# Kernel optimization log

Hardware: AMD Instinct MI355X
Metric: run time of the kernel (lower is better)

The kernel has to match this reference:

```python
import jax, jax.numpy as jnp
import numpy as np

NG, NF, NW = 5, 10, 8
STEP = NG + NF + 1          # 16 signatures per writer
MARGIN = 1.0
MODEL_LAMBDA = 0.01
GAMMA = 5.0                 # SoftDTW gamma from the module
BIG = 1e9                   # finite 'inf' so vjp stays NaN-free


def _pairwise_sq(x):
    # x: [B, N, F] -> squared-euclidean self-distance matrices [B, N, N]
    sq = jnp.sum(x * x, axis=-1)
    return sq[:, :, None] + sq[:, None, :] - 2.0 * jnp.einsum('bnf,bmf->bnm', x, x)


def _softdtw_diag_table(D):
    # Anti-diagonal Soft-DTW DP over all B matrices at once.
    # Returns all DP diagonals Rall[k, b, i] = R[i, k-i] so we can read
    # R[L-1, L-1] for each per-signature length L.
    B, N, _ = D.shape
    ii = jnp.arange(N)
    ks = jnp.arange(2 * N - 1)
    jidx = ks[:, None] - ii[None, :]                 # [2N-1, N] column index per diag
    valid = (jidx >= 0) & (jidx < N)
    jcl = jnp.clip(jidx, 0, N - 1)
    Ddiag = D[:, ii[None, :], jcl]                   # [B, 2N-1, N]
    Ddiag = jnp.transpose(Ddiag, (1, 0, 2))          # [2N-1, B, N]
    Ddiag = jnp.where(valid[:, None, :], Ddiag, 0.0)

    def shift(v):  # shift along i (last axis), pad with BIG
        return jnp.concatenate([jnp.full_like(v[:, :1], BIG), v[:, :-1]], axis=1)

    def softmin(a, b, c):
        return -GAMMA * jax.nn.logsumexp(jnp.stack([a, b, c]) * (-1.0 / GAMMA), axis=0)

    # k = 0: only cell (0,0): R = D[0,0] (softmin(0, inf, inf) = 0)
    R0 = jnp.where(ii[None, :] == 0, Ddiag[0], BIG)  # [B, N]
    Rm2_init = jnp.full_like(R0, BIG)

    def step(carry, inp):
        Rm2, Rm1 = carry
        Dk, vk = inp
        # cell (i, k-i): deps (i-1,j-1)=Rm2[i-1], (i-1,j)=Rm1[i-1], (i,j-1)=Rm1[i]
        Rk = Dk + softmin(shift(Rm2), shift(Rm1), Rm1)
        Rk = jnp.where(vk[None, :], Rk, BIG)
        return (Rm1, Rk), Rk

    _, Rs = jax.lax.scan(step, (Rm2_init, R0), (Ddiag[1:], valid[1:]))
    return jnp.concatenate([R0[None], Rs], axis=0)   # [2N-1, B, N]


def _forward(data, lens):
    B, N, _ = data.shape
    L = jnp.clip(lens.astype(jnp.int32), 1, N)       # valid prefix length per signature
    D = _pairwise_sq(data)                           # [B, N, N]
    Rall = _softdtw_diag_table(D)                    # [2N-1, B, N]
    # sdtw(x[:L], x[:L]) == R[L-1, L-1], found on diagonal k=2L-2 at position L-1
    sdtw_self = Rall[2 * L - 2, jnp.arange(B), L - 1]
    dists = sdtw_self / (2.0 * L.astype(data.dtype))  # /(len+len)

    d = dists.reshape(NW, STEP)
    dm = (d[:, :, None] + d[:, None, :]) * 0.5       # [NW, STEP, STEP]
    g = NG + 1
    dmg = dm[:, :g, :g]
    # scores[w,j,a,b] = relu(dm[w,j,a] + margin - dm[w,j,g+b]); lks[j] = max scalar
    scores = jax.nn.relu(dmg[:, :, :, None] + MARGIN - dm[:, :g, g:][:, :, None, :])
    maxj = jnp.max(scores, axis=(2, 3))              # [NW, g]
    sum_lks = jnp.sum(maxj, axis=1) * (g * NF)       # lks[j] broadcast over (g, nf)
    nnz = jnp.sum((maxj != 0).astype(data.dtype), axis=1) * (g * NF)
    lv = sum_lks / (nnz + 1.0)
    tril = jnp.tril(jnp.ones((g, g), dtype=bool), k=-1)
    only_pos = jnp.sum(jnp.where(tril[None], dmg, 0.0), axis=(1, 2)) * (MODEL_LAMBDA / NG)
    return jnp.sum(lv + only_pos) / NW


def setup_inputs() -> dict:
    key = jax.random.key(0)
    k1, k2 = jax.random.split(key)
    B = NW * STEP                                    # 128
    data = jax.random.normal(k1, (B, 512, 32), dtype=jnp.float32)
    lens = jax.random.randint(k2, (B,), 64, 513, dtype=jnp.int32)
    return {"data": data, "lens": lens}


def reference(data, lens):
    return _forward(data, lens)
```

## Files before the change

### kernel.cpp

```cpp
#include <hip/hip_runtime.h>
#include <stdint.h>

#define NGK   5
#define NFK   10
#define NWK   8
#define STEPW 16
#define NSEQ  512
#define FDIM  32
#define NBAT  128
#define SROWS 576
#define DEPTH 12
#define NR2   319
#define BIGV  1000000000.0f

#define INVGL 0.28853900817779268f
#define GLN2  3.4657359027997265f

#define EXP2F(x) __builtin_amdgcn_exp2f(x)
#define LOG2F(x) __builtin_amdgcn_logf(x)

typedef short bf16x8 __attribute__((ext_vector_type(8)));
typedef float f32x4  __attribute__((ext_vector_type(4)));
union U32F { uint32_t u; float f; };

__device__ __forceinline__ uint32_t f2bf(float f) {
    U32F c; c.f = f;
    return (c.u + 0x7FFFu + ((c.u >> 16) & 1u)) >> 16;
}
__device__ __forceinline__ float bflo(uint32_t u) { U32F c; c.u = u << 16; return c.f; }
__device__ __forceinline__ float bfhi(uint32_t u) { U32F c; c.u = u & 0xFFFF0000u; return c.f; }

__device__ __forceinline__ float dpp_shr1_f(float v) {
    U32F c; c.f = v;
    c.u = (uint32_t)__builtin_amdgcn_update_dpp(0, (int)c.u, 0x138, 0xF, 0xF, true);
    return c.f;
}

__global__ __launch_bounds__(256, 1) void prep_kernel(
    const float* __restrict__ data, uint16_t* __restrict__ xbf,
    float* __restrict__ sq)
{
    __shared__ uint32_t LB[NSEQ * 16];
    const int b = blockIdx.x;
    const int t = threadIdx.x;
    const float4* xb4 = (const float4*)(data + (size_t)b * (NSEQ * FDIM));
    uint2* xg = (uint2*)(xbf + (size_t)b * (NSEQ * FDIM));

    #pragma unroll
    for (int it = 0; it < 16; ++it) {
        int q = it * 256 + t;
        float4 v = xb4[q];
        uint32_t u0 = f2bf(v.x) | (f2bf(v.y) << 16);
        uint32_t u1 = f2bf(v.z) | (f2bf(v.w) << 16);
        LB[q * 2] = u0; LB[q * 2 + 1] = u1;
        uint2 st; st.x = u0; st.y = u1;
        xg[q] = st;
    }
    __syncthreads();
    #pragma unroll
    for (int rr = 0; rr < 2; ++rr) {
        int r = t + rr * 256;
        float acc = 0.f;
        #pragma unroll
        for (int c = 0; c < 16; ++c) {
            uint32_t u = LB[r * 16 + c];
            float lo = bflo(u), hi = bfhi(u);
            acc = fmaf(lo, lo, acc);
            acc = fmaf(hi, hi, acc);
        }
        sq[(size_t)b * NSEQ + r] = acc;
    }
}

__global__ __launch_bounds__(256, 1) void dgen2_kernel(
    const uint16_t* __restrict__ xbf, const float* __restrict__ sq,
    const int* __restrict__ lens, uint16_t* __restrict__ wsk)
{
    const int tj = blockIdx.x, b = blockIdx.y;
    int L = lens[b]; L = L < 1 ? 1 : (L > NSEQ ? NSEQ : L);
    const int lout = (L - 1) >> 3;
    const int maxS = ((L - 1) + 2 * lout) >> 1;
    if (tj * 16 > 2 * maxS + 1) return;

    const int t = threadIdx.x;
    const int w = t >> 6, lane = t & 63, rl = lane & 15, kq = lane >> 4, rr0 = kq * 4;
    const int j = tj * 16 + rl;

    const short* xb  = (const short*)(xbf + (size_t)b * (NSEQ * FDIM));
    const float* sqb = sq + (size_t)b * NSEQ;
    uint16_t* wb = wsk + (size_t)b * (NR2 * 1024);

    bf16x8 bfrag = *(const bf16x8*)(xb + j * FDIM + kq * 8);
    float sqJ = sqb[j];
    const bool jok = j < L;
    const int q0 = rr0 & 7;
    const int ladd = rr0 >> 3;

    for (int it = 0; it < 8; ++it) {
        int ti = w * 8 + it;
        if (tj * 16 + 4 * ti > 2 * maxS + 1) break;
        bf16x8 afrag = *(const bf16x8*)(xb + (ti * 16 + rl) * FDIM + kq * 8);
        f32x4 c = {0.f, 0.f, 0.f, 0.f};
        c = __builtin_amdgcn_mfma_f32_16x16x32_bf16(afrag, bfrag, c, 0, 0, 0);
        f32x4 s4 = *(const f32x4*)(sqb + ti * 16 + rr0);
        float wv[4];
        #pragma unroll
        for (int q2 = 0; q2 < 4; ++q2) {
            int i = ti * 16 + rr0 + q2;
            float dv = s4[q2] + sqJ - 2.f * c[q2];
            float e = EXP2F(-INVGL * dv);
            wv[q2] = (jok && (i < L)) ? e : 0.f;
        }
        int l  = ti * 2 + ladd;
        int cc = j + 2 * l;
        int S  = cc >> 1, sub = cc & 1;
        if (S <= maxS) {
            uint2 st;
            st.x = f2bf(wv[0]) | (f2bf(wv[1]) << 16);
            st.y = f2bf(wv[2]) | (f2bf(wv[3]) << 16);
            *(uint2*)(wb + (size_t)S * 1024 + l * 16 + sub * 8 + q0) = st;
        }
    }
}

__global__ __launch_bounds__(64, 1) void dp2_kernel(
    const uint16_t* __restrict__ wsk, const int* __restrict__ lens,
    float* __restrict__ dists, uint32_t* __restrict__ ctr,
    float* __restrict__ out)
{
    const int b = blockIdx.x, wl = threadIdx.x;
    const uint16_t* wb = wsk + (size_t)b * (NR2 * 1024) + wl * 16;
    int L = lens[b]; L = L < 1 ? 1 : (L > NSEQ ? NSEQ : L);
    const int lout = (L - 1) >> 3, qout = (L - 1) & 7;
    const int cout = (L - 1) + 2 * lout;
    const int S_out = cout >> 1;

#define ISSUE2(QA, QB, row) {                                                 \
    int gl_ = (row); if (gl_ > NR2 - 1) gl_ = NR2 - 1;                        \
    const uint16_t* pg_ = wb + (size_t)gl_ * 1024;                            \
    asm volatile("global_load_dwordx4 %0, %2, off\n\t"                        \
                 "global_load_dwordx4 %1, %2, off offset:16"                  \
                 : "=&v"(QA), "=&v"(QB) : "v"(pg_));                          \
}

    uint4 A0r, B0r, A1r, B1r, A2r, B2r, A3r, B3r,
          A4r, B4r, A5r, B5r, A6r, B6r, A7r, B7r;
    ISSUE2(A0r, B0r, 0) ISSUE2(A1r, B1r, 1) ISSUE2(A2r, B2r, 2) ISSUE2(A3r, B3r, 3)
    ISSUE2(A4r, B4r, 4) ISSUE2(A5r, B5r, 5) ISSUE2(A6r, B6r, 6) ISSUE2(A7r, B7r, 7)

    float E0 = 0.f, E1 = 0.f, E2 = 0.f, E3 = 0.f,
          E4 = 0.f, E5 = 0.f, E6 = 0.f, E7 = 0.f;
    float f0 = 0.f, f1 = 0.f, f2 = 0.f, f3 = 0.f,
          f4 = 0.f, f5 = 0.f, f6 = 0.f, f7 = 0.f;
    float ap  = (wl == 0) ? 1.0f : 0.f;
    float f7p = 0.f;

    int s = 0;

#define DSTEP(QA, QB) {                                                       \
    asm volatile("s_waitcnt vmcnt(14)" ::: "memory");                         \
    __builtin_amdgcn_sched_barrier(0);                                        \
    float wa0 = bflo(QA.x), wa1 = bfhi(QA.x), wa2 = bflo(QA.y), wa3 = bfhi(QA.y); \
    float wa4 = bflo(QA.z), wa5 = bfhi(QA.z), wa6 = bflo(QA.w), wa7 = bfhi(QA.w); \
    float wb0 = bflo(QB.x), wb1 = bfhi(QB.x), wb2 = bflo(QB.y), wb3 = bfhi(QB.y); \
    float wb4 = bflo(QB.z), wb5 = bfhi(QB.z), wb6 = bflo(QB.w), wb7 = bfhi(QB.w); \
    ISSUE2(QA, QB, s + 8);                                                    \
    float buA = dpp_shr1_f(f7p);                                              \
    float buB = dpp_shr1_f(E7);                                               \
    float a0 = (ap + E0) * wa0, a1 = (E0 + E1) * wa1;                         \
    float a2 = (E1 + E2) * wa2, a3 = (E2 + E3) * wa3;                         \
    float a4 = (E3 + E4) * wa4, a5 = (E4 + E5) * wa5;                         \
    float a6 = (E5 + E6) * wa6, a7 = (E6 + E7) * wa7;                         \
    f0 = fmaf(buA, wa0, a0);                                                  \
    f1 = fmaf(f0, wa1, a1);                                                   \
    f2 = fmaf(f1, wa2, a2);                                                   \
    f3 = fmaf(f2, wa3, a3);                                                   \
    f4 = fmaf(f3, wa4, a4);                                                   \
    f5 = fmaf(f4, wa5, a5);                                                   \
    f6 = fmaf(f5, wa6, a6);                                                   \
    f7 = fmaf(f6, wa7, a7);                                                   \
    float b0 = (buA + f0) * wb0, b1 = (f0 + f1) * wb1;                        \
    float b2 = (f1 + f2) * wb2, b3 = (f2 + f3) * wb3;                         \
    float b4 = (f3 + f4) * wb4, b5 = (f4 + f5) * wb5;                         \
    float b6 = (f5 + f6) * wb6, b7 = (f6 + f7) * wb7;                         \
    E0 = fmaf(buB, wb0, b0);                                                  \
    E1 = fmaf(E0, wb1, b1);                                                   \
    E2 = fmaf(E1, wb2, b2);                                                   \
    E3 = fmaf(E2, wb3, b3);                                                   \
    E4 = fmaf(E3, wb4, b4);                                                   \
    E5 = fmaf(E4, wb5, b5);                                                   \
    E6 = fmaf(E5, wb6, b6);                                                   \
    E7 = fmaf(E6, wb7, b7);                                                   \
    ap = buB; f7p = f7; ++s;                                                  \
}

    for (;;) {
        DSTEP(A0r, B0r); if (s > S_out) break;
        DSTEP(A1r, B1r); if (s > S_out) break;
        DSTEP(A2r, B2r); if (s > S_out) break;
        DSTEP(A3r, B3r); if (s > S_out) break;
        DSTEP(A4r, B4r); if (s > S_out) break;
        DSTEP(A5r, B5r); if (s > S_out) break;
        DSTEP(A6r, B6r); if (s > S_out) break;
        DSTEP(A7r, B7r); if (s > S_out) break;
    }
#undef DSTEP
#undef ISSUE2
    asm volatile("s_waitcnt vmcnt(0)" ::: "memory");

    if (wl == lout) {
        float eo;
        if ((cout & 1) == 0) {
            eo = f0;
            if (qout == 1) eo = f1; if (qout == 2) eo = f2; if (qout == 3) eo = f3;
            if (qout == 4) eo = f4; if (qout == 5) eo = f5; if (qout == 6) eo = f6;
            if (qout == 7) eo = f7;
        } else {
            eo = E0;
            if (qout == 1) eo = E1; if (qout == 2) eo = E2; if (qout == 3) eo = E3;
            if (qout == 4) eo = E4; if (qout == 5) eo = E5; if (qout == 6) eo = E6;
            if (qout == 7) eo = E7;
        }
        float dv = -GLN2 * LOG2F(eo) * (0.5f / (float)L);
        __hip_atomic_store(&dists[b], dv, __ATOMIC_RELEASE, __HIP_MEMORY_SCOPE_AGENT);
    }

    int old = 0;
    if (wl == 0) {
        old = (int)__hip_atomic_fetch_add(ctr, 1u, __ATOMIC_ACQ_REL,
                                          __HIP_MEMORY_SCOPE_AGENT);
    }
    old = __shfl(old, 0);
    if (old == NBAT - 1) {
        const int g = NGK + 1;
        float part = 0.f;
        if (wl < NWK) {
            float dd[STEPW];
            #pragma unroll
            for (int s2 = 0; s2 < STEPW; ++s2)
                dd[s2] = __hip_atomic_load(&dists[wl * STEPW + s2],
                                           __ATOMIC_RELAXED, __HIP_MEMORY_SCOPE_AGENT);
            float sum_lks = 0.f, nnz = 0.f;
            for (int ii = 0; ii < g; ++ii) {
                float mx = 0.f;
                for (int jj = 0; jj < g; ++jj) {
                    float dmg_ij = 0.5f * (dd[ii] + dd[jj]);
                    for (int f = 0; f < NFK; ++f) {
                        float sc = dmg_ij + 1.0f - 0.5f * (dd[ii] + dd[g + f]);
                        sc = fmaxf(sc, 0.f);
                        mx = fmaxf(mx, sc);
                    }
                }
                sum_lks += mx;
                nnz += (mx != 0.f) ? 1.f : 0.f;
            }
            sum_lks *= (float)(g * NFK);
            nnz     *= (float)(g * NFK);
            float lv = sum_lks / (nnz + 1.f);
            float only_pos = 0.f;
            for (int ii = 1; ii < g; ++ii)
                for (int jj = 0; jj < ii; ++jj)
                    only_pos += 0.5f * (dd[ii] + dd[jj]);
            only_pos *= (0.01f / (float)NGK);
            part = lv + only_pos;
        }
        float tot = 0.f;
        #pragma unroll
        for (int w2 = 0; w2 < NWK; ++w2) tot += __shfl(part, w2);
        if (wl == 0) out[0] = tot * (1.0f / (float)NWK);
    }
}

__global__ __launch_bounds__(256, 1) void dgen_kernel(
    const uint16_t* __restrict__ xbf, const float* __restrict__ sq,
    const int* __restrict__ lens, uint16_t* __restrict__ wsk)
{
    const int tj = blockIdx.x, b = blockIdx.y;
    int L = lens[b]; L = L < 1 ? 1 : (L > NSEQ ? NSEQ : L);
    const int smax = (L - 1) + ((L - 1) >> 3);
    int maxrow = smax + 8; if (maxrow > SROWS - 1) maxrow = SROWS - 1;
    if (tj * 16 > maxrow) return;

    const int t = threadIdx.x;
    const int w = t >> 6, lane = t & 63, rl = lane & 15, kq = lane >> 4, rr0 = kq * 4;
    const int j = tj * 16 + rl;

    const short* xb  = (const short*)(xbf + (size_t)b * (NSEQ * FDIM));
    const float* sqb = sq + (size_t)b * NSEQ;
    uint16_t* wb = wsk + (size_t)b * (SROWS * NSEQ);

    bf16x8 bfrag = *(const bf16x8*)(xb + j * FDIM + kq * 8);
    float sqJ = sqb[j];
    const bool jok = j < L;

    for (int it = 0; it < 8; ++it) {
        int ti = w * 8 + it;
        if (tj * 16 + ti * 2 > maxrow) break;
        bf16x8 afrag = *(const bf16x8*)(xb + (ti * 16 + rl) * FDIM + kq * 8);
        f32x4 c = {0.f, 0.f, 0.f, 0.f};
        c = __builtin_amdgcn_mfma_f32_16x16x32_bf16(afrag, bfrag, c, 0, 0, 0);
        f32x4 s4 = *(const f32x4*)(sqb + ti * 16 + rr0);
        float wv[4];
        #pragma unroll
        for (int q2 = 0; q2 < 4; ++q2) {
            int i = ti * 16 + rr0 + q2;
            float dv = s4[q2] + sqJ - 2.f * c[q2];
            float e = EXP2F(-INVGL * dv);
            wv[q2] = (jok && (i < L)) ? e : 0.f;
        }
        int sr = j + ti * 2 + (rr0 >> 3);
        uint2 st;
        st.x = f2bf(wv[0]) | (f2bf(wv[1]) << 16);
        st.y = f2bf(wv[2]) | (f2bf(wv[3]) << 16);
        *(uint2*)(wb + (size_t)sr * NSEQ + ti * 16 + rr0) = st;
    }
}

__global__ __launch_bounds__(64, 1) void dp_kernel(
    const uint16_t* __restrict__ wsk, const int* __restrict__ lens,
    float* __restrict__ dists, uint32_t* __restrict__ ctr,
    float* __restrict__ out)
{
    const int b = blockIdx.x, wl = threadIdx.x;
    const uint16_t* wb = wsk + (size_t)b * (SROWS * NSEQ) + wl * 8;
    int L = lens[b]; L = L < 1 ? 1 : (L > NSEQ ? NSEQ : L);
    const int lout = (L - 1) >> 3, qout = (L - 1) & 7, smax = (L - 1) + lout;

#define ISSUE(Q, row) {                                                       \
    int gl_ = (row); if (gl_ > SROWS - 1) gl_ = SROWS - 1;                    \
    const uint16_t* pg_ = wb + (size_t)gl_ * NSEQ;                            \
    asm volatile("global_load_dwordx4 %0, %1, off" : "=&v"(Q) : "v"(pg_));    \
}

    uint4 Q0, Q1, Q2, Q3, Q4, Q5, Q6, Q7, Q8, Q9, Qa, Qb;
    ISSUE(Q0, 0)  ISSUE(Q1, 1)  ISSUE(Q2, 2)  ISSUE(Q3, 3)
    ISSUE(Q4, 4)  ISSUE(Q5, 5)  ISSUE(Q6, 6)  ISSUE(Q7, 7)
    ISSUE(Q8, 8)  ISSUE(Q9, 9)  ISSUE(Qa, 10) ISSUE(Qb, 11)

    float E0 = 0.f, E1 = 0.f, E2 = 0.f, E3 = 0.f,
          E4 = 0.f, E5 = 0.f, E6 = 0.f, E7 = 0.f;
    float ap = (wl == 0) ? 1.0f : 0.f;

    int s = 0;

#define PHASE(Q) {                                                            \
    asm volatile("s_waitcnt vmcnt(11)" ::: "memory");                         \
    __builtin_amdgcn_sched_barrier(0);                                        \
    float w0 = bflo(Q.x), w1 = bfhi(Q.x), w2 = bflo(Q.y), w3 = bfhi(Q.y);     \
    float w4 = bflo(Q.z), w5 = bfhi(Q.z), w6 = bflo(Q.w), w7 = bfhi(Q.w);     \
    ISSUE(Q, s + DEPTH);                                                      \
    float bu = dpp_shr1_f(E7);                                                \
    float A0 = (ap + E0) * w0, A1 = (E0 + E1) * w1;                           \
    float A2 = (E1 + E2) * w2, A3 = (E2 + E3) * w3;                           \
    float A4 = (E3 + E4) * w4, A5 = (E4 + E5) * w5;                           \
    float A6 = (E5 + E6) * w6, A7 = (E6 + E7) * w7;                           \
    E0 = fmaf(bu, w0, A0);                                                    \
    E1 = fmaf(E0, w1, A1);                                                    \
    E2 = fmaf(E1, w2, A2);                                                    \
    E3 = fmaf(E2, w3, A3);                                                    \
    E4 = fmaf(E3, w4, A4);                                                    \
    E5 = fmaf(E4, w5, A5);                                                    \
    E6 = fmaf(E5, w6, A6);                                                    \
    E7 = fmaf(E6, w7, A7);                                                    \
    ap = bu; ++s;                                                             \
}

    for (;;) {
        PHASE(Q0); if (s > smax) break;
        PHASE(Q1); if (s > smax) break;
        PHASE(Q2); if (s > smax) break;
        PHASE(Q3); if (s > smax) break;
        PHASE(Q4); if (s > smax) break;
        PHASE(Q5); if (s > smax) break;
        PHASE(Q6); if (s > smax) break;
        PHASE(Q7); if (s > smax) break;
        PHASE(Q8); if (s > smax) break;
        PHASE(Q9); if (s > smax) break;
        PHASE(Qa); if (s > smax) break;
        PHASE(Qb); if (s > smax) break;
    }
#undef PHASE
#undef ISSUE
    asm volatile("s_waitcnt vmcnt(0)" ::: "memory");

    if (wl == lout) {
        float eo = E0;
        if (qout == 1) eo = E1; if (qout == 2) eo = E2; if (qout == 3) eo = E3;
        if (qout == 4) eo = E4; if (qout == 5) eo = E5; if (qout == 6) eo = E6;
        if (qout == 7) eo = E7;
        float dv = -GLN2 * LOG2F(eo) * (0.5f / (float)L);
        __hip_atomic_store(&dists[b], dv, __ATOMIC_RELEASE, __HIP_MEMORY_SCOPE_AGENT);
    }

    int old = 0;
    if (wl == 0) {
        old = (int)__hip_atomic_fetch_add(ctr, 1u, __ATOMIC_ACQ_REL,
                                          __HIP_MEMORY_SCOPE_AGENT);
    }
    old = __shfl(old, 0);
    if (old == NBAT - 1) {
        const int g = NGK + 1;
        float part = 0.f;
        if (wl < NWK) {
            float dd[STEPW];
            #pragma unroll
            for (int s2 = 0; s2 < STEPW; ++s2)
                dd[s2] = __hip_atomic_load(&dists[wl * STEPW + s2],
                                           __ATOMIC_RELAXED, __HIP_MEMORY_SCOPE_AGENT);
            float sum_lks = 0.f, nnz = 0.f;
            for (int ii = 0; ii < g; ++ii) {
                float mx = 0.f;
                for (int jj = 0; jj < g; ++jj) {
                    float dmg_ij = 0.5f * (dd[ii] + dd[jj]);
                    for (int f = 0; f < NFK; ++f) {
                        float sc = dmg_ij + 1.0f - 0.5f * (dd[ii] + dd[g + f]);
                        sc = fmaxf(sc, 0.f);
                        mx = fmaxf(mx, sc);
                    }
                }
                sum_lks += mx;
                nnz += (mx != 0.f) ? 1.f : 0.f;
            }
            sum_lks *= (float)(g * NFK);
            nnz     *= (float)(g * NFK);
            float lv = sum_lks / (nnz + 1.f);
            float only_pos = 0.f;
            for (int ii = 1; ii < g; ++ii)
                for (int jj = 0; jj < ii; ++jj)
                    only_pos += 0.5f * (dd[ii] + dd[jj]);
            only_pos *= (0.01f / (float)NGK);
            part = lv + only_pos;
        }
        float tot = 0.f;
        #pragma unroll
        for (int w2 = 0; w2 < NWK; ++w2) tot += __shfl(part, w2);
        if (wl == 0) out[0] = tot * (1.0f / (float)NWK);
    }
}

#define FXSTR 36
__global__ __launch_bounds__(512, 1) void sdtw_fb(
    const float* __restrict__ data, const int* __restrict__ lens,
    float* __restrict__ dists)
{
    __shared__ __align__(16) float LX[NSEQ * FXSTR];
    __shared__ float LSQ[NSEQ];
    __shared__ float RB[3][NSEQ + 2];

    const int b = blockIdx.x;
    const int t = threadIdx.x;
    const float* xb = data + (size_t)b * (NSEQ * FDIM);

    #pragma unroll
    for (int r = 0; r < 8; ++r) {
        int q = r * 512 + t;
        int j = q >> 3, c4 = (q & 7) << 2;
        float4 v = ((const float4*)xb)[q];
        *(float4*)&LX[j * FXSTR + c4] = v;
    }
    for (int idx = t; idx < 3 * (NSEQ + 2); idx += 512) ((float*)RB)[idx] = BIGV;
    __syncthreads();

    const int i = t;
    float4 xi[8];
    float sqi = 0.f;
    {
        const float* src = &LX[i * FXSTR];
        #pragma unroll
        for (int c = 0; c < 8; ++c) {
            float4 v = *(const float4*)&src[c * 4];
            xi[c] = v;
            sqi += v.x * v.x + v.y * v.y + v.z * v.z + v.w * v.w;
        }
        LSQ[i] = sqi;
    }
    int L = lens[b];
    L = L < 1 ? 1 : (L > NSEQ ? NSEQ : L);
    __syncthreads();

    float lastR = 0.0f;
    if (i == 0) {
        float dot = 0.f;
        #pragma unroll
        for (int c = 0; c < 8; ++c) {
            float4 v = xi[c];
            dot += v.x * v.x + v.y * v.y + v.z * v.z + v.w * v.w;
        }
        float d00 = sqi + sqi - 2.f * dot;
        lastR = d00;
        RB[0][1] = d00;
    }
    __syncthreads();

    float* b0 = RB[1]; float* b1 = RB[0]; float* b2 = RB[2];
    const int kend = 2 * L - 2;
    for (int k = 1; k <= kend; ++k) {
        int j = k - i;
        if (j >= 0 && j < L && i < L) {
            const float* xj = &LX[j * FXSTR];
            float d0 = 0.f, d1 = 0.f, d2 = 0.f, d3 = 0.f;
            #pragma unroll
            for (int c = 0; c < 8; ++c) {
                float4 v = *(const float4*)&xj[c * 4];
                d0 = fmaf(v.x, xi[c].x, d0);
                d1 = fmaf(v.y, xi[c].y, d1);
                d2 = fmaf(v.z, xi[c].z, d2);
                d3 = fmaf(v.w, xi[c].w, d3);
            }
            float dot = (d0 + d1) + (d2 + d3);
            float Dij = sqi + LSQ[j] - 2.f * dot;
            float a = b2[i], bb = b1[i], cc = b1[i + 1];
            float m = fminf(fminf(a, bb), cc);
            float e = EXP2F((m - a) * INVGL) + EXP2F((m - bb) * INVGL)
                    + EXP2F((m - cc) * INVGL);
            float r = Dij + m - GLN2 * LOG2F(e);
            b0[i + 1] = r;
            lastR = r;
        }
        __syncthreads();
        float* tmp = b2; b2 = b1; b1 = b0; b0 = tmp;
    }
    if (i == L - 1) dists[b] = lastR / (2.0f * (float)L);
}

__global__ __launch_bounds__(64) void finalize_kernel(
    const float* __restrict__ dists, float* __restrict__ out)
{
    __shared__ float acc[NWK];
    const int t = threadIdx.x;
    const int g = NGK + 1;
    if (t < NWK) {
        float dd[STEPW];
        #pragma unroll
        for (int s = 0; s < STEPW; ++s) dd[s] = dists[t * STEPW + s];

        float sum_lks = 0.f, nnz = 0.f;
        for (int ii = 0; ii < g; ++ii) {
            float mx = 0.f;
            for (int jj = 0; jj < g; ++jj) {
                float dmg_ij = 0.5f * (dd[ii] + dd[jj]);
                for (int f = 0; f < NFK; ++f) {
                    float s = dmg_ij + 1.0f - 0.5f * (dd[ii] + dd[g + f]);
                    s = fmaxf(s, 0.f);
                    mx = fmaxf(mx, s);
                }
            }
            sum_lks += mx;
            nnz += (mx != 0.f) ? 1.f : 0.f;
        }
        sum_lks *= (float)(g * NFK);
        nnz     *= (float)(g * NFK);
        float lv = sum_lks / (nnz + 1.f);

        float only_pos = 0.f;
        for (int ii = 1; ii < g; ++ii)
            for (int jj = 0; jj < ii; ++jj)
                only_pos += 0.5f * (dd[ii] + dd[jj]);
        only_pos *= (0.01f / (float)NGK);

        acc[t] = lv + only_pos;
    }
    __syncthreads();
    if (t == 0) {
        float s = 0.f;
        #pragma unroll
        for (int w = 0; w < NWK; ++w) s += acc[w];
        out[0] = s * (1.0f / (float)NWK);
    }
}

extern "C" void kernel_launch(void* const* d_in, const int* in_sizes, int n_in,
                              void* d_out, int out_size, void* d_ws, size_t ws_size,
                              hipStream_t stream)
{
    const float* data = (const float*)d_in[0];
    const int*   lens = (const int*)d_in[1];
    float* out   = (float*)d_out;
    float* dists = (float*)d_ws;
    uint32_t* ctr = (uint32_t*)((char*)d_ws + 512);

    const size_t OFF_XBF = 1024;
    const size_t OFF_SQ  = OFF_XBF + (size_t)NBAT * NSEQ * FDIM * 2;
    const size_t OFF_WSK = OFF_SQ  + (size_t)NBAT * NSEQ * 4;
    const size_t NEED2   = OFF_WSK + (size_t)NBAT * NR2 * 1024 * 2;
    const size_t NEED1   = OFF_WSK + (size_t)NBAT * SROWS * NSEQ * 2;

    if (ws_size >= NEED2) {
        uint16_t* xbf = (uint16_t*)((char*)d_ws + OFF_XBF);
        float*    sq  = (float*)((char*)d_ws + OFF_SQ);
        uint16_t* wsk = (uint16_t*)((char*)d_ws + OFF_WSK);
        hipMemsetAsync(ctr, 0, 4, stream);
        prep_kernel<<<NBAT, 256, 0, stream>>>(data, xbf, sq);
        dgen2_kernel<<<dim3(32, NBAT), 256, 0, stream>>>(xbf, sq, lens, wsk);
        dp2_kernel<<<NBAT, 64, 0, stream>>>(wsk, lens, dists, ctr, out);
    } else if (ws_size >= NEED1) {
        uint16_t* xbf = (uint16_t*)((char*)d_ws + OFF_XBF);
        float*    sq  = (float*)((char*)d_ws + OFF_SQ);
        uint16_t* wsk = (uint16_t*)((char*)d_ws + OFF_WSK);
        hipMemsetAsync(ctr, 0, 4, stream);
        prep_kernel<<<NBAT, 256, 0, stream>>>(data, xbf, sq);
        dgen_kernel<<<dim3(32, NBAT), 256, 0, stream>>>(xbf, sq, lens, wsk);
        dp_kernel<<<NBAT, 64, 0, stream>>>(wsk, lens, dists, ctr, out);
    } else {
        sdtw_fb<<<NBAT, 512, 0, stream>>>(data, lens, dists);
        finalize_kernel<<<1, 64, 0, stream>>>(dists, out);
    }
}
```

Before: 82.87 us.

## Split soft-DTW wavefront DP across two waves with LDS handoff and pipelined lag

Adds dgen3/dp3 kernels that split each sequence's anti-diagonal DP over two 64-lane waves, each covering 256 rows. Wave 1 trails wave 0 by a fixed lag and takes its boundary values through an LDS slot array, with a block barrier after each group of eight steps. The weight workspace is re-laid out per wave to match. The goal is to shorten the serial critical path per block by halving the per-lane chain length. Counter reset moves from a memset into prep_kernel, which removes one launch. The cost is a barrier per phase and extra pipeline-fill steps.

```diff
diff --git a/kernel.cpp b/kernel.cpp
--- a/kernel.cpp
+++ b/kernel.cpp
@@ -11,6 +11,7 @@
 #define SROWS 576
 #define DEPTH 12
 #define NR2   319
+#define NS3   320
 #define BIGV  1000000000.0f
 
 #define INVGL 0.28853900817779268f
@@ -38,11 +39,13 @@
 
 __global__ __launch_bounds__(256, 1) void prep_kernel(
     const float* __restrict__ data, uint16_t* __restrict__ xbf,
-    float* __restrict__ sq)
+    float* __restrict__ sq, uint32_t* __restrict__ ctr)
 {
     __shared__ uint32_t LB[NSEQ * 16];
     const int b = blockIdx.x;
     const int t = threadIdx.x;
+    if (b == 0 && t == 0)
+        __hip_atomic_store(ctr, 0u, __ATOMIC_RELEASE, __HIP_MEMORY_SCOPE_AGENT);
     const float4* xb4 = (const float4*)(data + (size_t)b * (NSEQ * FDIM));
     uint2* xg = (uint2*)(xbf + (size_t)b * (NSEQ * FDIM));
 
@@ -69,6 +72,196 @@
             acc = fmaf(hi, hi, acc);
         }
         sq[(size_t)b * NSEQ + r] = acc;
+    }
+}
+
+__global__ __launch_bounds__(256, 1) void dgen3_kernel(
+    const uint16_t* __restrict__ xbf, const float* __restrict__ sq,
+    const int* __restrict__ lens, uint16_t* __restrict__ wsk)
+{
+    const int tj = blockIdx.x, b = blockIdx.y;
+    int L = lens[b]; L = L < 1 ? 1 : (L > NSEQ ? NSEQ : L);
+    const int GUARD = ((L - 1) >> 1) + 64;
+    if (tj * 8 > GUARD) return;
+
+    const int t = threadIdx.x;
+    const int w4 = t >> 6, lane = t & 63, rl = lane & 15, kq = lane >> 4, rr0 = kq * 4;
+    const int j = tj * 16 + rl;
+
+    const short* xb  = (const short*)(xbf + (size_t)b * (NSEQ * FDIM));
+    const float* sqb = sq + (size_t)b * NSEQ;
+    uint16_t* wb = wsk + (size_t)b * (NS3 * 1024);
+
+    bf16x8 bfrag = *(const bf16x8*)(xb + j * FDIM + kq * 8);
+    float sqJ = sqb[j];
+    const bool jok = j < L;
+
+    for (int it = 0; it < 8; ++it) {
+        int ti = w4 * 8 + it;
+        int smin = tj * 8 + (ti & 15) * 4;
+        if (smin > GUARD) break;
+        bf16x8 afrag = *(const bf16x8*)(xb + (ti * 16 + rl) * FDIM + kq * 8);
+        f32x4 c = {0.f, 0.f, 0.f, 0.f};
+        c = __builtin_amdgcn_mfma_f32_16x16x32_bf16(afrag, bfrag, c, 0, 0, 0);
+        f32x4 s4 = *(const f32x4*)(sqb + ti * 16 + rr0);
+        float wv4[4];
+        #pragma unroll
+        for (int q2 = 0; q2 < 4; ++q2) {
+            int i = ti * 16 + rr0 + q2;
+            float dv = s4[q2] + sqJ - 2.f * c[q2];
+            float e = EXP2F(-INVGL * dv);
+            wv4[q2] = (jok && (i < L)) ? e : 0.f;
+        }
+        int i0 = ti * 16 + rr0;
+        int wv = i0 >> 8, l = (i0 & 255) >> 2;
+        int cc = j + 2 * l;
+        int s = cc >> 1, sub = cc & 1;
+        if (s <= GUARD) {
+            uint2 st;
+            st.x = f2bf(wv4[0]) | (f2bf(wv4[1]) << 16);
+            st.y = f2bf(wv4[2]) | (f2bf(wv4[3]) << 16);
+            *(uint2*)(wb + (size_t)((s * 2 + wv) * 64 + l) * 8 + sub * 4) = st;
+        }
+    }
+}
+
+__global__ __launch_bounds__(128, 1) void dp3_kernel(
+    const uint16_t* __restrict__ wsk, const int* __restrict__ lens,
+    float* __restrict__ dists, uint32_t* __restrict__ ctr,
+    float* __restrict__ out)
+{
+    __shared__ float2 SLOT[256];
+
+    const int b = blockIdx.x;
+    const int t = threadIdx.x;
+    const int wv = t >> 6, wl = t & 63;
+
+    int L = lens[b]; L = L < 1 ? 1 : (L > NSEQ ? NSEQ : L);
+    const int ow = (L - 1) >> 8, ol = ((L - 1) & 255) >> 2, oq = (L - 1) & 3;
+    const int sout = ((L - 1) + 2 * ol) >> 1;
+    const int cpar = ((L - 1) + 2 * ol) & 1;
+    const bool mine = (ow == wv);
+    const int swend = ((L - 1) + 126) >> 1;
+    const int pmax  = swend >> 3;
+    const int NP    = pmax + 10;
+
+    const uint16_t* wlane = wsk + (size_t)b * (NS3 * 1024) + wv * 512 + wl * 8;
+    const bool takeslot = (wv == 1) && (wl == 0);
+
+#define ISS(Q, row) {                                                         \
+    int r_ = (row); r_ = r_ > swend ? swend : r_;                             \
+    const uint16_t* p_ = wlane + (size_t)r_ * 1024;                           \
+    asm volatile("global_load_dwordx4 %0, %1, off" : "=&v"(Q) : "v"(p_));     \
+}
+
+    uint4 Q0, Q1, Q2, Q3, Q4, Q5, Q6, Q7;
+    ISS(Q0, 0) ISS(Q1, 1) ISS(Q2, 2) ISS(Q3, 3)
+    ISS(Q4, 4) ISS(Q5, 5) ISS(Q6, 6) ISS(Q7, 7)
+
+    float E0 = 0.f, E1 = 0.f, E2 = 0.f, E3 = 0.f;
+    float f0 = 0.f, f1 = 0.f, f2 = 0.f, f3 = 0.f;
+    float ap  = (wv == 0 && wl == 0) ? 1.0f : 0.f;
+    float f3p = 0.f;
+    float eo  = 0.f;
+    int s = 0;
+
+#define PH3(Q) {                                                              \
+    asm volatile("s_waitcnt vmcnt(7)" ::: "memory");        \
+    __builtin_amdgcn_sched_barrier(0);                                        \
+    float WA0 = bflo(Q.x), WA1 = bfhi(Q.x), WA2 = bflo(Q.y), WA3 = bfhi(Q.y); \
+    float WB0 = bflo(Q.z), WB1 = bfhi(Q.z), WB2 = bflo(Q.w), WB3 = bfhi(Q.w); \
+    ISS(Q, s + 8);                                                            \
+    float2 sl = SLOT[s < 256 ? s : 255];                                      \
+    float buA = dpp_shr1_f(f3p);                                              \
+    float buB = dpp_shr1_f(E3);                                               \
+    buA = takeslot ? sl.x : buA;                                              \
+    buB = takeslot ? sl.y : buB;                                              \
+    float a0 = (ap + E0) * WA0;  f0 = fmaf(buA, WA0, a0);                     \
+    float a1 = (E0 + E1) * WA1;  f1 = fmaf(f0, WA1, a1);                      \
+    float a2 = (E1 + E2) * WA2;  f2 = fmaf(f1, WA2, a2);                      \
+    float a3 = (E2 + E3) * WA3;  f3 = fmaf(f2, WA3, a3);                      \
+    float b0 = (buA + f0) * WB0; E0 = fmaf(buB, WB0, b0);                     \
+    float b1 = (f0 + f1) * WB1;  E1 = fmaf(E0, WB1, b1);                      \
+    float b2 = (f1 + f2) * WB2;  E2 = fmaf(E1, WB2, b2);                      \
+    float b3 = (f2 + f3) * WB3;  E3 = fmaf(E2, WB3, b3);                      \
+    if (wv == 0 && wl == 63 && s >= 63 && s <= swend) {                       \
+        float2 sv; sv.x = f3; sv.y = E3; SLOT[s - 63] = sv;                   \
+    }                                                                         \
+    if (mine && s == sout) {                                                  \
+        float ea = f0; if (oq == 1) ea = f1; if (oq == 2) ea = f2;            \
+        if (oq == 3) ea = f3;                                                 \
+        float eb = E0; if (oq == 1) eb = E1; if (oq == 2) eb = E2;            \
+        if (oq == 3) eb = E3;                                                 \
+        eo = cpar ? eb : ea;                                                  \
+    }                                                                         \
+    ap = buB; f3p = f3; ++s;                                                  \
+}
+
+    for (int p = 0; p < NP; ++p) {
+        const bool active = (wv == 0) ? (p <= pmax)
+                                      : (p >= 9 && p <= pmax + 9);
+        if (active) {
+            PH3(Q0); PH3(Q1); PH3(Q2); PH3(Q3);
+            PH3(Q4); PH3(Q5); PH3(Q6); PH3(Q7);
+        }
+        asm volatile("s_waitcnt lgkmcnt(0)" ::: "memory");
+        __builtin_amdgcn_s_barrier();
+    }
+#undef PH3
+#undef ISS
+    asm volatile("s_waitcnt vmcnt(0)" ::: "memory");
+
+    if (mine && wl == ol) {
+        float dv = -GLN2 * LOG2F(eo) * (0.5f / (float)L);
+        __hip_atomic_store(&dists[b], dv, __ATOMIC_RELEASE, __HIP_MEMORY_SCOPE_AGENT);
+    }
+    __syncthreads();
+
+    if (wv == 0) {
+        int old = 0;
+        if (wl == 0) {
+            old = (int)__hip_atomic_fetch_add(ctr, 1u, __ATOMIC_ACQ_REL,
+                                              __HIP_MEMORY_SCOPE_AGENT);
+        }
+        old = __shfl(old, 0);
+        if (old == NBAT - 1) {
+            const int g = NGK + 1;
+            float part = 0.f;
+            if (wl < NWK) {
+                float dd[STEPW];
+                #pragma unroll
+                for (int s2 = 0; s2 < STEPW; ++s2)
+                    dd[s2] = __hip_atomic_load(&dists[wl * STEPW + s2],
+                                               __ATOMIC_RELAXED, __HIP_MEMORY_SCOPE_AGENT);
+                float sum_lks = 0.f, nnz = 0.f;
+                for (int ii = 0; ii < g; ++ii) {
+                    float mx = 0.f;
+                    for (int jj = 0; jj < g; ++jj) {
+                        float dmg_ij = 0.5f * (dd[ii] + dd[jj]);
+                        for (int f = 0; f < NFK; ++f) {
+                            float sc = dmg_ij + 1.0f - 0.5f * (dd[ii] + dd[g + f]);
+                            sc = fmaxf(sc, 0.f);
+                            mx = fmaxf(mx, sc);
+                        }
+                    }
+                    sum_lks += mx;
+                    nnz += (mx != 0.f) ? 1.f : 0.f;
+                }
+                sum_lks *= (float)(g * NFK);
+                nnz     *= (float)(g * NFK);
+                float lv = sum_lks / (nnz + 1.f);
+                float only_pos = 0.f;
+                for (int ii = 1; ii < g; ++ii)
+                    for (int jj = 0; jj < ii; ++jj)
+                        only_pos += 0.5f * (dd[ii] + dd[jj]);
+                only_pos *= (0.01f / (float)NGK);
+                part = lv + only_pos;
+            }
+            float tot = 0.f;
+            #pragma unroll
+            for (int w2 = 0; w2 < NWK; ++w2) tot += __shfl(part, w2);
+            if (wl == 0) out[0] = tot * (1.0f / (float)NWK);
+        }
     }
 }
 
@@ -271,173 +464,6 @@
     }
 }
 
-__global__ __launch_bounds__(256, 1) void dgen_kernel(
-    const uint16_t* __restrict__ xbf, const float* __restrict__ sq,
-    const int* __restrict__ lens, uint16_t* __restrict__ wsk)
-{
-    const int tj = blockIdx.x, b = blockIdx.y;
-    int L = lens[b]; L = L < 1 ? 1 : (L > NSEQ ? NSEQ : L);
-    const int smax = (L - 1) + ((L - 1) >> 3);
-    int maxrow = smax + 8; if (maxrow > SROWS - 1) maxrow = SROWS - 1;
-    if (tj * 16 > maxrow) return;
-
-    const int t = threadIdx.x;
-    const int w = t >> 6, lane = t & 63, rl = lane & 15, kq = lane >> 4, rr0 = kq * 4;
-    const int j = tj * 16 + rl;
-
-    const short* xb  = (const short*)(xbf + (size_t)b * (NSEQ * FDIM));
-    const float* sqb = sq + (size_t)b * NSEQ;
-    uint16_t* wb = wsk + (size_t)b * (SROWS * NSEQ);
-
-    bf16x8 bfrag = *(const bf16x8*)(xb + j * FDIM + kq * 8);
-    float sqJ = sqb[j];
-    const bool jok = j < L;
-
-    for (int it = 0; it < 8; ++it) {
-        int ti = w * 8 + it;
-        if (tj * 16 + ti * 2 > maxrow) break;
-        bf16x8 afrag = *(const bf16x8*)(xb + (ti * 16 + rl) * FDIM + kq * 8);
-        f32x4 c = {0.f, 0.f, 0.f, 0.f};
-        c = __builtin_amdgcn_mfma_f32_16x16x32_bf16(afrag, bfrag, c, 0, 0, 0);
-        f32x4 s4 = *(const f32x4*)(sqb + ti * 16 + rr0);
-        float wv[4];
-        #pragma unroll
-        for (int q2 = 0; q2 < 4; ++q2) {
-            int i = ti * 16 + rr0 + q2;
-            float dv = s4[q2] + sqJ - 2.f * c[q2];
-            float e = EXP2F(-INVGL * dv);
-            wv[q2] = (jok && (i < L)) ? e : 0.f;
-        }
-        int sr = j + ti * 2 + (rr0 >> 3);
-        uint2 st;
-        st.x = f2bf(wv[0]) | (f2bf(wv[1]) << 16);
-        st.y = f2bf(wv[2]) | (f2bf(wv[3]) << 16);
-        *(uint2*)(wb + (size_t)sr * NSEQ + ti * 16 + rr0) = st;
-    }
-}
-
-__global__ __launch_bounds__(64, 1) void dp_kernel(
-    const uint16_t* __restrict__ wsk, const int* __restrict__ lens,
-    float* __restrict__ dists, uint32_t* __restrict__ ctr,
-    float* __restrict__ out)
-{
-    const int b = blockIdx.x, wl = threadIdx.x;
-    const uint16_t* wb = wsk + (size_t)b * (SROWS * NSEQ) + wl * 8;
-    int L = lens[b]; L = L < 1 ? 1 : (L > NSEQ ? NSEQ : L);
-    const int lout = (L - 1) >> 3, qout = (L - 1) & 7, smax = (L - 1) + lout;
-
-#define ISSUE(Q, row) {                                                       \
-    int gl_ = (row); if (gl_ > SROWS - 1) gl_ = SROWS - 1;                    \
-    const uint16_t* pg_ = wb + (size_t)gl_ * NSEQ;                            \
-    asm volatile("global_load_dwordx4 %0, %1, off" : "=&v"(Q) : "v"(pg_));    \
-}
-
-    uint4 Q0, Q1, Q2, Q3, Q4, Q5, Q6, Q7, Q8, Q9, Qa, Qb;
-    ISSUE(Q0, 0)  ISSUE(Q1, 1)  ISSUE(Q2, 2)  ISSUE(Q3, 3)
-    ISSUE(Q4, 4)  ISSUE(Q5, 5)  ISSUE(Q6, 6)  ISSUE(Q7, 7)
-    ISSUE(Q8, 8)  ISSUE(Q9, 9)  ISSUE(Qa, 10) ISSUE(Qb, 11)
-
-    float E0 = 0.f, E1 = 0.f, E2 = 0.f, E3 = 0.f,
-          E4 = 0.f, E5 = 0.f, E6 = 0.f, E7 = 0.f;
-    float ap = (wl == 0) ? 1.0f : 0.f;
-
-    int s = 0;
-
-#define PHASE(Q) {                                                            \
-    asm volatile("s_waitcnt vmcnt(11)" ::: "memory");                         \
-    __builtin_amdgcn_sched_barrier(0);                                        \
-    float w0 = bflo(Q.x), w1 = bfhi(Q.x), w2 = bflo(Q.y), w3 = bfhi(Q.y);     \
-    float w4 = bflo(Q.z), w5 = bfhi(Q.z), w6 = bflo(Q.w), w7 = bfhi(Q.w);     \
-    ISSUE(Q, s + DEPTH);                                                      \
-    float bu = dpp_shr1_f(E7);                                                \
-    float A0 = (ap + E0) * w0, A1 = (E0 + E1) * w1;                           \
-    float A2 = (E1 + E2) * w2, A3 = (E2 + E3) * w3;                           \
-    float A4 = (E3 + E4) * w4, A5 = (E4 + E5) * w5;                           \
-    float A6 = (E5 + E6) * w6, A7 = (E6 + E7) * w7;                           \
-    E0 = fmaf(bu, w0, A0);                                                    \
-    E1 = fmaf(E0, w1, A1);                                                    \
-    E2 = fmaf(E1, w2, A2);                                                    \
-    E3 = fmaf(E2, w3, A3);                                                    \
-    E4 = fmaf(E3, w4, A4);                                                    \
-    E5 = fmaf(E4, w5, A5);                                                    \
-    E6 = fmaf(E5, w6, A6);                                                    \
-    E7 = fmaf(E6, w7, A7);                                                    \
-    ap = bu; ++s;                                                             \
-}
-
-    for (;;) {
-        PHASE(Q0); if (s > smax) break;
-        PHASE(Q1); if (s > smax) break;
-        PHASE(Q2); if (s > smax) break;
-        PHASE(Q3); if (s > smax) break;
-        PHASE(Q4); if (s > smax) break;
-        PHASE(Q5); if (s > smax) break;
-        PHASE(Q6); if (s > smax) break;
-        PHASE(Q7); if (s > smax) break;
-        PHASE(Q8); if (s > smax) break;
-        PHASE(Q9); if (s > smax) break;
-        PHASE(Qa); if (s > smax) break;
-        PHASE(Qb); if (s > smax) break;
-    }
-#undef PHASE
-#undef ISSUE
-    asm volatile("s_waitcnt vmcnt(0)" ::: "memory");
-
-    if (wl == lout) {
-        float eo = E0;
-        if (qout == 1) eo = E1; if (qout == 2) eo = E2; if (qout == 3) eo = E3;
-        if (qout == 4) eo = E4; if (qout == 5) eo = E5; if (qout == 6) eo = E6;
-        if (qout == 7) eo = E7;
-        float dv = -GLN2 * LOG2F(eo) * (0.5f / (float)L);
-        __hip_atomic_store(&dists[b], dv, __ATOMIC_RELEASE, __HIP_MEMORY_SCOPE_AGENT);
-    }
-
-    int old = 0;
-    if (wl == 0) {
-        old = (int)__hip_atomic_fetch_add(ctr, 1u, __ATOMIC_ACQ_REL,
-                                          __HIP_MEMORY_SCOPE_AGENT);
-    }
-    old = __shfl(old, 0);
-    if (old == NBAT - 1) {
-        const int g = NGK + 1;
-        float part = 0.f;
-        if (wl < NWK) {
-            float dd[STEPW];
-            #pragma unroll
-            for (int s2 = 0; s2 < STEPW; ++s2)
-                dd[s2] = __hip_atomic_load(&dists[wl * STEPW + s2],
-                                           __ATOMIC_RELAXED, __HIP_MEMORY_SCOPE_AGENT);
-            float sum_lks = 0.f, nnz = 0.f;
-            for (int ii = 0; ii < g; ++ii) {
-                float mx = 0.f;
-                for (int jj = 0; jj < g; ++jj) {
-                    float dmg_ij = 0.5f * (dd[ii] + dd[jj]);
-                    for (int f = 0; f < NFK; ++f) {
-                        float sc = dmg_ij + 1.0f - 0.5f * (dd[ii] + dd[g + f]);
-                        sc = fmaxf(sc, 0.f);
-                        mx = fmaxf(mx, sc);
-                    }
-                }
-                sum_lks += mx;
-                nnz += (mx != 0.f) ? 1.f : 0.f;
-            }
-            sum_lks *= (float)(g * NFK);
-            nnz     *= (float)(g * NFK);
-            float lv = sum_lks / (nnz + 1.f);
-            float only_pos = 0.f;
-            for (int ii = 1; ii < g; ++ii)
-                for (int jj = 0; jj < ii; ++jj)
-                    only_pos += 0.5f * (dd[ii] + dd[jj]);
-            only_pos *= (0.01f / (float)NGK);
-            part = lv + only_pos;
-        }
-        float tot = 0.f;
-        #pragma unroll
-        for (int w2 = 0; w2 < NWK; ++w2) tot += __shfl(part, w2);
-        if (wl == 0) out[0] = tot * (1.0f / (float)NWK);
-    }
-}
-
 #define FXSTR 36
 __global__ __launch_bounds__(512, 1) void sdtw_fb(
     const float* __restrict__ data, const int* __restrict__ lens,
@@ -582,25 +608,23 @@
     const size_t OFF_XBF = 1024;
     const size_t OFF_SQ  = OFF_XBF + (size_t)NBAT * NSEQ * FDIM * 2;
     const size_t OFF_WSK = OFF_SQ  + (size_t)NBAT * NSEQ * 4;
+    const size_t NEED3   = OFF_WSK + (size_t)NBAT * NS3 * 1024 * 2;
     const size_t NEED2   = OFF_WSK + (size_t)NBAT * NR2 * 1024 * 2;
-    const size_t NEED1   = OFF_WSK + (size_t)NBAT * SROWS * NSEQ * 2;
-
-    if (ws_size >= NEED2) {
+
+    if (ws_size >= NEED3) {
         uint16_t* xbf = (uint16_t*)((char*)d_ws + OFF_XBF);
         float*    sq  = (float*)((char*)d_ws + OFF_SQ);
         uint16_t* wsk = (uint16_t*)((char*)d_ws + OFF_WSK);
-        hipMemsetAsync(ctr, 0, 4, stream);
-        prep_kernel<<<NBAT, 256, 0, stream>>>(data, xbf, sq);
-        dgen2_kernel<<<dim3(32, NBAT), 256, 0, stream>>>(xbf, sq, lens, wsk);
-        dp2_kernel<<<NBAT, 64, 0, stream>>>(wsk, lens, dists, ctr, out);
-    } else if (ws_size >= NEED1) {
+        prep_kernel<<<NBAT, 256, 0, stream>>>(data, xbf, sq, ctr);
+        dgen3_kernel<<<dim3(32, NBAT), 256, 0, stream>>>(xbf, sq, lens, wsk);
+        dp3_kernel<<<NBAT, 128, 0, stream>>>(wsk, lens, dists, ctr, out);
+    } else if (ws_size >= NEED2) {
         uint16_t* xbf = (uint16_t*)((char*)d_ws + OFF_XBF);
         float*    sq  = (float*)((char*)d_ws + OFF_SQ);
         uint16_t* wsk = (uint16_t*)((char*)d_ws + OFF_WSK);
-        hipMemsetAsync(ctr, 0, 4, stream);
-        prep_kernel<<<NBAT, 256, 0, stream>>>(data, xbf, sq);
-        dgen_kernel<<<dim3(32, NBAT), 256, 0, stream>>>(xbf, sq, lens, wsk);
-        dp_kernel<<<NBAT, 64, 0, stream>>>(wsk, lens, dists, ctr, out);
+        prep_kernel<<<NBAT, 256, 0, stream>>>(data, xbf, sq, ctr);
+        dgen2_kernel<<<dim3(32, NBAT), 256, 0, stream>>>(xbf, sq, lens, wsk);
+        dp2_kernel<<<NBAT, 64, 0, stream>>>(wsk, lens, dists, ctr, out);
     } else {
         sdtw_fb<<<NBAT, 512, 0, stream>>>(data, lens, dists);
         finalize_kernel<<<1, 64, 0, stream>>>(dists, out);
```

New measurement: 101.4 us. +22.3%, slower.
